# Optimization experiments

Measured on AMD Instinct MI355X. Metric: run time of the kernel, lower is better.

The kernel has to match this reference:

```python
import jax, jax.numpy as jnp
import numpy as np

DROP_P = 0.1  # module default dropout


def setup_inputs() -> dict:
    key = jax.random.key(0)
    kq, kk, kv = jax.random.split(key, 3)
    B, L, H = 4, 4096, 64
    return {
        "q": jax.random.normal(kq, (B, L, H), dtype=jnp.float32),
        "k": jax.random.normal(kk, (B, L, H), dtype=jnp.float32),
        "v": jax.random.normal(kv, (B, L, H), dtype=jnp.float32),
    }


def reference(q, k, v):
    # q: [B, ql, H], k: [B, kl, H], v: [B, kl, H]
    H = q.shape[-1]
    scale = 1.0 / jnp.sqrt(jnp.asarray(H, dtype=q.dtype))
    # [B, ql, kl] score matrix (materialized, as in the original module)
    scores = jnp.einsum('bqh,bkh->bqk', q, k) * scale
    ql, kl = scores.shape[1], scores.shape[2]
    causal = jnp.tril(jnp.ones((ql, kl), dtype=bool))  # self.tril[:ql, :kl]
    scores = jnp.where(causal[None, :, :], scores, -jnp.inf)
    wei = jax.nn.softmax(scores, axis=-1)
    # deterministic dropout (train-mode path in the torch module)
    keep_p = 1.0 - DROP_P
    keep = jax.random.bernoulli(jax.random.key(42), keep_p, wei.shape)
    wei = jnp.where(keep, wei / keep_p, jnp.zeros((), dtype=wei.dtype))
    return jnp.einsum('bqk,bkh->bqh', wei, v)
```

## Files before the change

### kernel.cpp

```cpp
#include <hip/hip_runtime.h>

#define LQ   4096
#define HDIM 64
#define KEEP_LIMIT (7549747u << 9)
#define SCALE_LOG2E 0.18033688011112042f

typedef __attribute__((ext_vector_type(8))) short short8v;
typedef __attribute__((ext_vector_type(4))) short short4v;
typedef __attribute__((ext_vector_type(4))) float f32x4;

__device__ __forceinline__ unsigned rotl32(unsigned x, int r) {
  return (x << r) | (x >> (32 - r));
}

__device__ __forceinline__ float keep_sel(unsigned j, float e) {
  const unsigned ks1 = 42u;
  const unsigned ks2 = 0x1BD11BDAu ^ 42u;
  unsigned x0 = 0u, x1 = j + ks1;
#define TFR(r) { x0 += x1; x1 = rotl32(x1, r); x1 ^= x0; }
  TFR(13) TFR(15) TFR(26) TFR(6)   x0 += ks1; x1 += ks2 + 1u;
  TFR(17) TFR(29) TFR(16) TFR(24)  x0 += ks2; x1 += 0u  + 2u;
  TFR(13) TFR(15) TFR(26) TFR(6)   x0 += 0u;  x1 += ks1 + 3u;
  TFR(17) TFR(29) TFR(16) TFR(24)  x0 += ks1; x1 += ks2 + 4u;
  TFR(13) TFR(15) TFR(26) TFR(6)   x0 += ks2; x1 += 0u  + 5u;
#undef TFR
  return ((x0 ^ x1) < KEEP_LIMIT) ? e : 0.f;
}

__device__ __forceinline__ unsigned short f2bf(float x) {
  unsigned u = __float_as_uint(x);
  u += 0x7fffu + ((u >> 16) & 1u);
  return (unsigned short)(u >> 16);
}

__device__ __forceinline__ void gload16(const void* g, void* l) {
  __builtin_amdgcn_global_load_lds(
      (const __attribute__((address_space(1))) unsigned int*)g,
      (__attribute__((address_space(3))) unsigned int*)l, 16, 0, 0);
}

#if __has_builtin(__builtin_amdgcn_mfma_f32_16x16x16bf16_1k)
#define MFMA16(a, b, c) __builtin_amdgcn_mfma_f32_16x16x16bf16_1k(a, b, c, 0, 0, 0)
#else
__device__ __forceinline__ f32x4 mfma16_asm(short4v a, short4v b, f32x4 c) {
  f32x4 d;
  asm volatile("v_mfma_f32_16x16x16_bf16 %0, %1, %2, %3"
               : "=v"(d) : "v"(a), "v"(b), "v"(c));
  return d;
}
#define MFMA16(a, b, c) mfma16_asm(a, b, c)
#endif

__global__ __launch_bounds__(256) void prep(const float* __restrict__ k,
                                            const float* __restrict__ v,
                                            unsigned short* __restrict__ kb,
                                            unsigned short* __restrict__ vtb) {
  __shared__ float t[64][65];
  const int b = blockIdx.y, tl = blockIdx.x;
  const int tid = threadIdx.x, lane = tid & 63, grp = tid >> 6;
  {
    const float* kp = k + ((size_t)b * LQ + tl * 64) * HDIM;
    unsigned short* kbp = kb + ((size_t)b * LQ + tl * 64) * HDIM;
#pragma unroll
    for (int i = 0; i < 4; i++) {
      int e = (i * 256 + tid) * 4;
      float4 x = *(const float4*)(kp + e);
      ushort4 y;
      y.x = f2bf(x.x); y.y = f2bf(x.y); y.z = f2bf(x.z); y.w = f2bf(x.w);
      *(ushort4*)(kbp + e) = y;
    }
  }
#pragma unroll
  for (int c = 0; c < 16; c++) {
    int r = c * 4 + grp;
    t[r][lane] = v[((size_t)b * LQ + tl * 64 + r) * HDIM + lane];
  }
  __syncthreads();
#pragma unroll
  for (int c = 0; c < 16; c++) {
    int h = c * 4 + grp;
    vtb[((size_t)b * HDIM + h) * LQ + tl * 64 + lane] = f2bf(t[lane][h]);
  }
}

__global__ __launch_bounds__(256, 8) void attn(
    const float* __restrict__ q, const unsigned short* __restrict__ kb,
    const unsigned short* __restrict__ vtb, float* __restrict__ o,
    float* __restrict__ plsum) {
  __shared__ __align__(16) unsigned short vl[2][64 * 64];

  const int bx = blockIdx.x;
  const int tile16 = 255 - (bx >> 3);
  const int b = (bx >> 1) & 3;
  const int s = bx & 1;
  const int tid = threadIdx.x, lane = tid & 63, wq = tid >> 6;
  const int g = lane >> 4, r = lane & 15;
  const int qrow = tile16 * 16 + r;
  const int nt = (tile16 >> 2) + 1;
  const int half = (nt + 1) >> 1;
  const int ts = s ? half : 0, te = s ? nt : half;
  const int ntm1 = nt - 1;
  const unsigned sw = (unsigned)((r & 7) << 4);

  short8v qf0, qf1;
  {
    const float* qp = q + ((size_t)b * LQ + qrow) * HDIM + g * 8;
    float4 a0 = *(const float4*)qp;
    float4 a1 = *(const float4*)(qp + 4);
    float4 b0 = *(const float4*)(qp + 32);
    float4 b1 = *(const float4*)(qp + 36);
    qf0[0] = (short)f2bf(a0.x); qf0[1] = (short)f2bf(a0.y);
    qf0[2] = (short)f2bf(a0.z); qf0[3] = (short)f2bf(a0.w);
    qf0[4] = (short)f2bf(a1.x); qf0[5] = (short)f2bf(a1.y);
    qf0[6] = (short)f2bf(a1.z); qf0[7] = (short)f2bf(a1.w);
    qf1[0] = (short)f2bf(b0.x); qf1[1] = (short)f2bf(b0.y);
    qf1[2] = (short)f2bf(b0.z); qf1[3] = (short)f2bf(b0.w);
    qf1[4] = (short)f2bf(b1.x); qf1[5] = (short)f2bf(b1.y);
    qf1[6] = (short)f2bf(b1.z); qf1[7] = (short)f2bf(b1.w);
  }

  const char* vt_b = (const char*)vtb + (size_t)b * HDIM * LQ * 2;
  unsigned vsrc0, vsrc1;
  {
    unsigned d0 = (unsigned)(tid * 16);
    unsigned d1 = d0 + 4096u;
    vsrc0 = (d0 >> 7) * (LQ * 2) + ((d0 & 127u) ^ (((d0 >> 7) & 7u) << 4));
    vsrc1 = (d1 >> 7) * (LQ * 2) + ((d1 & 127u) ^ (((d1 >> 7) & 7u) << 4));
  }
  const char* kbl =
      (const char*)kb + ((size_t)b * LQ + wq * 16 + r) * 128 + g * 16;

#define STAGE(T, BI)                                                           \
  {                                                                            \
    gload16(vt_b + vsrc0 + (size_t)(T) * 128,                                  \
            (char*)&vl[BI][0] + wq * 1024);                                    \
    gload16(vt_b + vsrc1 + (size_t)(T) * 128,                                  \
            (char*)&vl[BI][0] + wq * 1024 + 4096);                             \
  }

  f32x4 acc[4];
  acc[0] = (f32x4){0, 0, 0, 0}; acc[1] = (f32x4){0, 0, 0, 0};
  acc[2] = (f32x4){0, 0, 0, 0}; acc[3] = (f32x4){0, 0, 0, 0};
  float lsum = 0.f;

  short8v k0c, k1c;
  if (ts < te) {
    STAGE(ts, 0)
    k0c = *(const short8v*)(kbl + (size_t)ts * 8192);
    k1c = *(const short8v*)(kbl + (size_t)ts * 8192 + 64);
  }
  __syncthreads();

  for (int t = ts; t < te; ++t) {
    const int bi = (t - ts) & 1;
    short8v k0n, k1n;
    const bool more = (t + 1 < te);
    if (more) {
      STAGE(t + 1, bi ^ 1)
      k0n = *(const short8v*)(kbl + (size_t)(t + 1) * 8192);
      k1n = *(const short8v*)(kbl + (size_t)(t + 1) * 8192 + 64);
    }

    f32x4 S = __builtin_amdgcn_mfma_f32_16x16x32_bf16(k0c, qf0,
                                                      (f32x4){0, 0, 0, 0}, 0, 0, 0);
    S = __builtin_amdgcn_mfma_f32_16x16x32_bf16(k1c, qf1, S, 0, 0, 0);

    const int kvb = t * 64 + wq * 16 + g * 4;
    const unsigned jb =
        ((unsigned)b << 24) | ((unsigned)qrow << 12) | (unsigned)kvb;
    float w[4];
    if (t == ntm1) {
#pragma unroll
      for (int reg = 0; reg < 4; ++reg) {
        float e = (kvb + reg <= qrow) ? exp2f(S[reg] * SCALE_LOG2E) : 0.f;
        lsum += e;
        w[reg] = keep_sel(jb + (unsigned)reg, e);
      }
    } else {
#pragma unroll
      for (int reg = 0; reg < 4; ++reg) {
        float e = exp2f(S[reg] * SCALE_LOG2E);
        lsum += e;
        w[reg] = keep_sel(jb + (unsigned)reg, e);
      }
    }

    union { unsigned u[2]; short4v s4; } pu;
    asm("v_cvt_pk_bf16_f32 %0, %1, %2" : "=v"(pu.u[0]) : "v"(w[0]), "v"(w[1]));
    asm("v_cvt_pk_bf16_f32 %0, %1, %2" : "=v"(pu.u[1]) : "v"(w[2]), "v"(w[3]));
    const short4v pa = pu.s4;

    const char* vlp = (const char*)&vl[bi][0] + r * 128 +
                      (((unsigned)(wq * 32 + g * 8)) ^ sw);
#pragma unroll
    for (int hg = 0; hg < 4; ++hg) {
      short4v vf = *(const short4v*)(vlp + hg * 2048);
      acc[hg] = MFMA16(pa, vf, acc[hg]);
    }
    __syncthreads();
    if (more) { k0c = k0n; k1c = k1n; }
  }
#undef STAGE

  lsum += __shfl_xor(lsum, 16);
  lsum += __shfl_xor(lsum, 32);
  if (lane < 16)
    atomicAdd(&plsum[b * LQ + tile16 * 16 + lane], lsum);

  float* ob = o + ((size_t)b * LQ + tile16 * 16) * HDIM;
#pragma unroll
  for (int hg = 0; hg < 4; ++hg)
#pragma unroll
    for (int reg = 0; reg < 4; ++reg)
      atomicAdd(&ob[(g * 4 + reg) * HDIM + hg * 16 + r], acc[hg][reg]);
}

__global__ __launch_bounds__(256) void norm(float* __restrict__ o,
                                            const float* __restrict__ plsum) {
  const int idx = blockIdx.x * 256 + threadIdx.x;
  f32x4 x = ((const f32x4*)o)[idx];
  const float inv = 1.0f / (plsum[idx >> 4] * 0.9f);
  ((f32x4*)o)[idx] = x * inv;
}

extern "C" void kernel_launch(void* const* d_in, const int* in_sizes, int n_in,
                              void* d_out, int out_size, void* d_ws, size_t ws_size,
                              hipStream_t stream) {
  const float* q = (const float*)d_in[0];
  const float* k = (const float*)d_in[1];
  const float* v = (const float*)d_in[2];
  float* out = (float*)d_out;
  unsigned short* kb  = (unsigned short*)d_ws;
  unsigned short* vtb = kb + (size_t)4 * LQ * HDIM;
  float* plsum = (float*)((char*)d_ws + (size_t)4 * 1024 * 1024);

  hipMemsetAsync(out, 0, (size_t)4 * LQ * HDIM * sizeof(float), stream);
  hipMemsetAsync(plsum, 0, (size_t)4 * LQ * sizeof(float), stream);
  prep<<<dim3(64, 4), 256, 0, stream>>>(k, v, kb, vtb);
  attn<<<2048, 256, 0, stream>>>(q, kb, vtb, out, plsum);
  norm<<<1024, 256, 0, stream>>>(out, plsum);
}
```

Before: 108.4 us.

## Process two KV tiles per barrier with quad-buffered V staging

The attention loop now handles two 64-key tiles per iteration. It uses four LDS buffers so the next pair of V tiles and K fragments are prefetched while the current pair is computed, which halves the number of __syncthreads barriers. V fragments are loaded from LDS before the score MFMAs, and the launch-bounds occupancy hint drops from 8 to 4 blocks per CU. The trade-off is doubled LDS use and more registers, which may reduce occupancy in exchange for fewer syncs and more latency hiding.

New measurement: 96.67 us (median of 2 runs). 1.12x faster.

```diff
diff --git a/kernel.cpp b/kernel.cpp
--- a/kernel.cpp
+++ b/kernel.cpp
@@ -83,11 +83,11 @@
   }
 }
 
-__global__ __launch_bounds__(256, 8) void attn(
+__global__ __launch_bounds__(256, 4) void attn(
     const float* __restrict__ q, const unsigned short* __restrict__ kb,
     const unsigned short* __restrict__ vtb, float* __restrict__ o,
     float* __restrict__ plsum) {
-  __shared__ __align__(16) unsigned short vl[2][64 * 64];
+  __shared__ __align__(16) unsigned short vl[4][64 * 64];
 
   const int bx = blockIdx.x;
   const int tile16 = 255 - (bx >> 3);
@@ -101,6 +101,8 @@
   const int ts = s ? half : 0, te = s ? nt : half;
   const int ntm1 = nt - 1;
   const unsigned sw = (unsigned)((r & 7) << 4);
+  const unsigned jq = ((unsigned)b << 24) | ((unsigned)qrow << 12);
+  const f32x4 zero4 = (f32x4){0.f, 0.f, 0.f, 0.f};
 
   short8v qf0, qf1;
   {
@@ -120,87 +122,105 @@
   }
 
   const char* vt_b = (const char*)vtb + (size_t)b * HDIM * LQ * 2;
-  unsigned vsrc0, vsrc1;
+  const char* vpA;
+  const char* vpB;
   {
     unsigned d0 = (unsigned)(tid * 16);
     unsigned d1 = d0 + 4096u;
-    vsrc0 = (d0 >> 7) * (LQ * 2) + ((d0 & 127u) ^ (((d0 >> 7) & 7u) << 4));
-    vsrc1 = (d1 >> 7) * (LQ * 2) + ((d1 & 127u) ^ (((d1 >> 7) & 7u) << 4));
-  }
-  const char* kbl =
-      (const char*)kb + ((size_t)b * LQ + wq * 16 + r) * 128 + g * 16;
-
-#define STAGE(T, BI)                                                           \
+    unsigned vsrc0 = (d0 >> 7) * (LQ * 2) + ((d0 & 127u) ^ (((d0 >> 7) & 7u) << 4));
+    unsigned vsrc1 = (d1 >> 7) * (LQ * 2) + ((d1 & 127u) ^ (((d1 >> 7) & 7u) << 4));
+    vpA = vt_b + vsrc0 + (size_t)ts * 128;
+    vpB = vt_b + vsrc1 + (size_t)ts * 128;
+  }
+  const char* kp =
+      (const char*)kb + ((size_t)b * LQ + wq * 16 + r) * 128 + g * 16 +
+      (size_t)ts * 8192;
+
+  char* const lw = (char*)&vl[0][0] + wq * 1024;
+
+  f32x4 acc[4];
+  acc[0] = zero4; acc[1] = zero4; acc[2] = zero4; acc[3] = zero4;
+  float lsum = 0.f;
+
+  const int n = te - ts;
+  short8v kA0 = {}, kA1 = {}, kB0 = {}, kB1 = {};
+  if (n > 0) {
+    gload16(vpA, lw);
+    gload16(vpB, lw + 4096);
+    kA0 = *(const short8v*)(kp);
+    kA1 = *(const short8v*)(kp + 64);
+  }
+  if (n > 1) {
+    gload16(vpA + 128, lw + 8192);
+    gload16(vpB + 128, lw + 8192 + 4096);
+    kB0 = *(const short8v*)(kp + 8192);
+    kB1 = *(const short8v*)(kp + 8192 + 64);
+  }
+  kp += 16384;
+  __syncthreads();
+
+#define COMPUTE_TILE(K0, K1, BUFI, T, DIAG)                                    \
   {                                                                            \
-    gload16(vt_b + vsrc0 + (size_t)(T) * 128,                                  \
-            (char*)&vl[BI][0] + wq * 1024);                                    \
-    gload16(vt_b + vsrc1 + (size_t)(T) * 128,                                  \
-            (char*)&vl[BI][0] + wq * 1024 + 4096);                             \
-  }
-
-  f32x4 acc[4];
-  acc[0] = (f32x4){0, 0, 0, 0}; acc[1] = (f32x4){0, 0, 0, 0};
-  acc[2] = (f32x4){0, 0, 0, 0}; acc[3] = (f32x4){0, 0, 0, 0};
-  float lsum = 0.f;
-
-  short8v k0c, k1c;
-  if (ts < te) {
-    STAGE(ts, 0)
-    k0c = *(const short8v*)(kbl + (size_t)ts * 8192);
-    k1c = *(const short8v*)(kbl + (size_t)ts * 8192 + 64);
-  }
-  __syncthreads();
-
-  for (int t = ts; t < te; ++t) {
-    const int bi = (t - ts) & 1;
-    short8v k0n, k1n;
-    const bool more = (t + 1 < te);
-    if (more) {
-      STAGE(t + 1, bi ^ 1)
-      k0n = *(const short8v*)(kbl + (size_t)(t + 1) * 8192);
-      k1n = *(const short8v*)(kbl + (size_t)(t + 1) * 8192 + 64);
+    const char* vlp = (const char*)&vl[BUFI][0] + r * 128 +                    \
+                      (((unsigned)(wq * 32 + g * 8)) ^ sw);                    \
+    short4v vf[4];                                                             \
+    _Pragma("unroll") for (int hg = 0; hg < 4; ++hg)                           \
+        vf[hg] = *(const short4v*)(vlp + hg * 2048);                           \
+    f32x4 S = __builtin_amdgcn_mfma_f32_16x16x32_bf16(K0, qf0, zero4, 0, 0, 0);\
+    S = __builtin_amdgcn_mfma_f32_16x16x32_bf16(K1, qf1, S, 0, 0, 0);          \
+    const int kvb = (T) * 64 + wq * 16 + g * 4;                                \
+    float w[4];                                                                \
+    if (DIAG) {                                                                \
+      _Pragma("unroll") for (int reg = 0; reg < 4; ++reg) {                    \
+        float e = (kvb + reg <= qrow) ? exp2f(S[reg] * SCALE_LOG2E) : 0.f;     \
+        lsum += e;                                                             \
+        w[reg] = keep_sel(jq | (unsigned)(kvb + reg), e);                      \
+      }                                                                        \
+    } else {                                                                   \
+      _Pragma("unroll") for (int reg = 0; reg < 4; ++reg) {                    \
+        float e = exp2f(S[reg] * SCALE_LOG2E);                                 \
+        lsum += e;                                                             \
+        w[reg] = keep_sel(jq | (unsigned)(kvb + reg), e);                      \
+      }                                                                        \
+    }                                                                          \
+    union { unsigned u[2]; short4v s4; } pu;                                   \
+    asm("v_cvt_pk_bf16_f32 %0, %1, %2" : "=v"(pu.u[0]) : "v"(w[0]), "v"(w[1]));\
+    asm("v_cvt_pk_bf16_f32 %0, %1, %2" : "=v"(pu.u[1]) : "v"(w[2]), "v"(w[3]));\
+    const short4v pa = pu.s4;                                                  \
+    _Pragma("unroll") for (int hg = 0; hg < 4; ++hg)                           \
+        acc[hg] = MFMA16(pa, vf[hg], acc[hg]);                                 \
+  }
+
+  int t = ts;
+  int base = 0;
+  for (; t + 2 <= te; t += 2) {
+    short8v nA0 = kA0, nA1 = kA1, nB0 = kB0, nB1 = kB1;
+    char* const lwn = lw + (base ^ 2) * 8192;
+    if (t + 2 < te) {
+      gload16(vpA + 256, lwn);
+      gload16(vpB + 256, lwn + 4096);
+      nA0 = *(const short8v*)(kp);
+      nA1 = *(const short8v*)(kp + 64);
     }
-
-    f32x4 S = __builtin_amdgcn_mfma_f32_16x16x32_bf16(k0c, qf0,
-                                                      (f32x4){0, 0, 0, 0}, 0, 0, 0);
-    S = __builtin_amdgcn_mfma_f32_16x16x32_bf16(k1c, qf1, S, 0, 0, 0);
-
-    const int kvb = t * 64 + wq * 16 + g * 4;
-    const unsigned jb =
-        ((unsigned)b << 24) | ((unsigned)qrow << 12) | (unsigned)kvb;
-    float w[4];
-    if (t == ntm1) {
-#pragma unroll
-      for (int reg = 0; reg < 4; ++reg) {
-        float e = (kvb + reg <= qrow) ? exp2f(S[reg] * SCALE_LOG2E) : 0.f;
-        lsum += e;
-        w[reg] = keep_sel(jb + (unsigned)reg, e);
-      }
-    } else {
-#pragma unroll
-      for (int reg = 0; reg < 4; ++reg) {
-        float e = exp2f(S[reg] * SCALE_LOG2E);
-        lsum += e;
-        w[reg] = keep_sel(jb + (unsigned)reg, e);
-      }
+    if (t + 3 < te) {
+      gload16(vpA + 384, lwn + 8192);
+      gload16(vpB + 384, lwn + 8192 + 4096);
+      nB0 = *(const short8v*)(kp + 8192);
+      nB1 = *(const short8v*)(kp + 8192 + 64);
     }
 
-    union { unsigned u[2]; short4v s4; } pu;
-    asm("v_cvt_pk_bf16_f32 %0, %1, %2" : "=v"(pu.u[0]) : "v"(w[0]), "v"(w[1]));
-    asm("v_cvt_pk_bf16_f32 %0, %1, %2" : "=v"(pu.u[1]) : "v"(w[2]), "v"(w[3]));
-    const short4v pa = pu.s4;
-
-    const char* vlp = (const char*)&vl[bi][0] + r * 128 +
-                      (((unsigned)(wq * 32 + g * 8)) ^ sw);
-#pragma unroll
-    for (int hg = 0; hg < 4; ++hg) {
-      short4v vf = *(const short4v*)(vlp + hg * 2048);
-      acc[hg] = MFMA16(pa, vf, acc[hg]);
-    }
+    COMPUTE_TILE(kA0, kA1, base, t, false)
+    COMPUTE_TILE(kB0, kB1, base + 1, t + 1, (t + 1) == ntm1)
+
     __syncthreads();
-    if (more) { k0c = k0n; k1c = k1n; }
-  }
-#undef STAGE
+    kA0 = nA0; kA1 = nA1; kB0 = nB0; kB1 = nB1;
+    vpA += 256; vpB += 256; kp += 16384;
+    base ^= 2;
+  }
+  if (t < te) {
+    COMPUTE_TILE(kA0, kA1, base, t, t == ntm1)
+  }
+#undef COMPUTE_TILE
 
   lsum += __shfl_xor(lsum, 16);
   lsum += __shfl_xor(lsum, 32);
```
